# Optimization experiments

Measured on AMD Instinct MI355X. Metric: run time of the kernel, lower is better.

Reference implementation:

```python
import jax, jax.numpy as jnp
import numpy as np

N_WIN, P, C = 2048, 64, 256      # total windows, tokens per window (8x8 partition), channels
M_SEL, KEEP, REAL = 1536, 48, 40 # selected windows, topk tokens kept per window, real (non-padded)
H, DH = 8, 32                    # heads, dim_head
EPS = 1e-5


def _ln(x, g, b):
    mu = jnp.mean(x, axis=-1, keepdims=True)
    v = jnp.mean(jnp.square(x - mu), axis=-1, keepdims=True)
    return (x - mu) * jax.lax.rsqrt(v + EPS) * g + b


def setup_inputs() -> dict:
    key = jax.random.key(0)
    ks = jax.random.split(key, 6)
    rng = np.random.default_rng(0)
    # distinct selected windows
    index_window = jnp.asarray(np.sort(rng.choice(N_WIN, size=M_SEL, replace=False)), jnp.int32)
    # per selected window: 48 distinct token positions out of 64; first 40 real, last 8 padded
    pos = np.argsort(rng.random((M_SEL, P)), axis=1)[:, :KEEP]
    tok = np.arange(M_SEL)[:, None] * P + pos           # flat rows into (M*P, C)
    index_token = jnp.asarray(tok.reshape(-1), jnp.int32)
    asy_index = jnp.asarray(tok[:, :REAL].reshape(-1), jnp.int32)
    padding_index = jnp.asarray(tok[:, REAL:].reshape(-1), jnp.int32)
    w = lambda k, s: jax.random.normal(k, s, jnp.float32) * 0.02
    return {
        "x": jax.random.normal(ks[0], (N_WIN, P, C), jnp.float32),
        "qkv_w": w(ks[1], (C, 3 * C)), "qkv_b": jnp.zeros((3 * C,), jnp.float32),
        "proj_w": w(ks[2], (C, C)), "proj_b": jnp.zeros((C,), jnp.float32),
        "norm1_g": jnp.ones((C,), jnp.float32), "norm1_b": jnp.zeros((C,), jnp.float32),
        "norm2_g": jnp.ones((C,), jnp.float32), "norm2_b": jnp.zeros((C,), jnp.float32),
        "ls1_g": jnp.full((C,), 1e-5, jnp.float32), "ls2_g": jnp.full((C,), 1e-5, jnp.float32),
        "mlp_w1": w(ks[3], (C, 4 * C)), "mlp_b1": jnp.zeros((4 * C,), jnp.float32),
        "mlp_w2": w(ks[4], (4 * C, C)), "mlp_b2": jnp.zeros((C,), jnp.float32),
        "index_window": index_window, "index_token": index_token,
        "padding_index": padding_index, "asy_index": asy_index,
        "M": M_SEL,
    }


def reference(x, qkv_w, qkv_b, proj_w, proj_b, norm1_g, norm1_b, norm2_g, norm2_b,
              ls1_g, ls2_g, mlp_w1, mlp_b1, mlp_w2, mlp_b2,
              index_window, index_token, padding_index, asy_index, M):
    scale = DH ** -0.5
    x1 = _ln(x, norm1_g, norm1_b)                       # norm1 over all windows (N,P,C)
    X = x1
    XX = x1[index_window].reshape(-1, C)                # gather selected windows -> (M*P, C)
    XX = XX.at[asy_index].set(_ln(XX[asy_index], norm2_g, norm2_b))
    shortcut = XX[asy_index]
    xt = XX[index_token].reshape(M, KEEP, C)            # gather kept tokens per window
    qkv = (xt @ qkv_w + qkv_b).reshape(M, KEEP, H, 3 * DH).transpose(0, 2, 1, 3)
    q, k, v = jnp.split(qkv, 3, axis=-1)                # each (M,H,KEEP,DH)
    attn = jnp.einsum('mhqd,mhkd->mhqk', q, k) * scale  # (M,H,Q,K)
    # scatter scores into full map keyed by KEY token row, mask padded keys, gather back
    am = attn.transpose(0, 3, 2, 1).reshape(M * KEEP, KEEP, H)
    attn_map = jnp.zeros((M * P, KEEP, H), attn.dtype)
    attn_map = attn_map.at[index_token].set(am)
    attn_map = attn_map.at[padding_index].set(-10000.0)
    attn = attn_map[index_token].reshape(M, KEEP, KEEP, H).transpose(0, 3, 2, 1)
    attn = jax.nn.softmax(attn, axis=-1)
    out = jnp.einsum('mhqk,mhkd->mhqd', attn, v).transpose(0, 2, 1, 3).reshape(M, KEEP, C)
    out = out @ proj_w + proj_b
    XX = XX.at[index_token].set(out.reshape(-1, C))
    xa = shortcut + XX[asy_index] * ls1_g               # residual + LayerScale
    hdn = jax.nn.gelu(xa @ mlp_w1 + mlp_b1, approximate=False)
    xa = xa + (hdn @ mlp_w2 + mlp_b2) * ls2_g           # (enable_CB=False path)
    XX = XX.at[asy_index].set(xa)
    Xw = X[index_window].reshape(-1, C)
    XX = XX.at[padding_index].set(Xw[padding_index])    # restore padded rows
    X = X.at[index_window].set(XX.reshape(M, P, C))     # scatter windows back
    return X
```

## Files before the change

### kernel.cpp

```cpp
#include <hip/hip_runtime.h>

typedef __attribute__((ext_vector_type(8))) short bf16x8;
typedef __attribute__((ext_vector_type(4))) float f32x4;
typedef unsigned short u16;
typedef unsigned int u32;
typedef unsigned char u8;

#define NWIN 2048
#define P 64
#define C 256
#define MSEL 1536
#define KEEP 48
#define REAL 40
#define H 8
#define DH 32
#define MROWS (MSEL * REAL)

#define B_WQKVT   0
#define B_W1T     393216
#define B_PROJT8  917504
#define B_W2T8    983040
#define B_INV     1245184
#define B_ABUF    1769472
#define B_XA      33226752
#define B_QKV8    64684032
#define B_ATTNO8  111869952
#define B_H8      64684032

__device__ __forceinline__ u16 f2bf(float f) {
    u32 u = __float_as_uint(f);
    u += 0x7FFF + ((u >> 16) & 1);
    return (u16)(u >> 16);
}
__device__ __forceinline__ float bf2f(u16 h) { return __uint_as_float(((u32)h) << 16); }
__device__ __forceinline__ u8 f2fp8(float f) {
    return (u8)__builtin_amdgcn_cvt_pk_fp8_f32(f, 0.0f, 0, false);
}

__global__ __launch_bounds__(256) void prep_weights(const float* __restrict__ qkv_w,
                                                    const float* __restrict__ proj_w,
                                                    const float* __restrict__ w1,
                                                    const float* __restrict__ w2,
                                                    u8* __restrict__ ws) {
    int i = blockIdx.x * 256 + threadIdx.x;
    if (i < 196608) {
        int n = i >> 8, k = i & 255;
        ((u16*)(ws + B_WQKVT))[i] = f2bf(qkv_w[k * 768 + n]);
    } else if (i < 458752) {
        int j = i - 196608; int n = j >> 8, k = j & 255;
        ((u16*)(ws + B_W1T))[j] = f2bf(w1[k * 1024 + n]);
    } else if (i < 524288) {
        int j = i - 458752; int n = j >> 8, k = j & 255;
        (ws + B_PROJT8)[j] = f2fp8(proj_w[k * 256 + n]);
    } else if (i < 786432) {
        int j = i - 524288; int n = j >> 10, k = j & 1023;
        (ws + B_W2T8)[j] = f2fp8(w2[k * 256 + n]);
    } else {
        ((int*)(ws + B_INV))[i - 786432] = -1;
    }
}

__global__ __launch_bounds__(256) void build_inv(const int* __restrict__ asy,
                                                 const int* __restrict__ iwin,
                                                 int* __restrict__ inv) {
    int r = blockIdx.x * 256 + threadIdx.x;
    int flat = asy[r];
    inv[iwin[flat >> 6] * P + (flat & 63)] = r;
}

__global__ __launch_bounds__(256) void ln12_kernel(const float* __restrict__ x,
                                                   const float* __restrict__ g1,
                                                   const float* __restrict__ b1,
                                                   const float* __restrict__ g2,
                                                   const float* __restrict__ b2,
                                                   const int* __restrict__ inv,
                                                   float* __restrict__ out,
                                                   u16* __restrict__ Abuf) {
    int row = blockIdx.x * 4 + (threadIdx.x >> 6);
    int l = threadIdx.x & 63;
    const float4 v = *(const float4*)(x + (size_t)row * C + l * 4);
    float s = v.x + v.y + v.z + v.w;
    float q = v.x * v.x + v.y * v.y + v.z * v.z + v.w * v.w;
    #pragma unroll
    for (int m = 1; m < 64; m <<= 1) { s += __shfl_xor(s, m); q += __shfl_xor(q, m); }
    float mu = s * (1.0f / C);
    float rs = rsqrtf(q * (1.0f / C) - mu * mu + 1e-5f);
    float4 gg = *(const float4*)(g1 + l * 4);
    float4 bb = *(const float4*)(b1 + l * 4);
    float4 o;
    o.x = (v.x - mu) * rs * gg.x + bb.x;
    o.y = (v.y - mu) * rs * gg.y + bb.y;
    o.z = (v.z - mu) * rs * gg.z + bb.z;
    o.w = (v.w - mu) * rs * gg.w + bb.w;
    *(float4*)(out + (size_t)row * C + l * 4) = o;
    int r = inv[row];
    if (r >= 0) {
        float s2 = o.x + o.y + o.z + o.w;
        float q2 = o.x * o.x + o.y * o.y + o.z * o.z + o.w * o.w;
        #pragma unroll
        for (int m = 1; m < 64; m <<= 1) { s2 += __shfl_xor(s2, m); q2 += __shfl_xor(q2, m); }
        float mu2 = s2 * (1.0f / C);
        float rs2 = rsqrtf(q2 * (1.0f / C) - mu2 * mu2 + 1e-5f);
        float4 g2v = *(const float4*)(g2 + l * 4);
        float4 b2v = *(const float4*)(b2 + l * 4);
        ushort4 ob;
        ob.x = f2bf((o.x - mu2) * rs2 * g2v.x + b2v.x);
        ob.y = f2bf((o.y - mu2) * rs2 * g2v.y + b2v.y);
        ob.z = f2bf((o.z - mu2) * rs2 * g2v.z + b2v.z);
        ob.w = f2bf((o.w - mu2) * rs2 * g2v.w + b2v.w);
        *(ushort4*)(Abuf + (size_t)r * C + l * 4) = ob;
    }
}

template <int N, int K, class Epi>
__global__ __launch_bounds__(256) void gemm_bt(const u16* __restrict__ A,
                                               const u16* __restrict__ B, Epi epi,
                                               int chunk) {
    constexpr int NB = N / 128;
    int bid = blockIdx.x;
    bid = (bid & 7) * chunk + (bid >> 3);
    int bm = bid / NB, bn = bid % NB;
    __shared__ u16 lA[128 * 64], lB[128 * 64];
    int t = threadIdx.x;
    int l = t & 63, w = t >> 6;
    int wr = w >> 1, wc = w & 1;
    int l15 = l & 15, g4 = l >> 4;
    int xr = l15 & 7;

    f32x4 acc[4][4];
    #pragma unroll
    for (int a = 0; a < 4; a++)
        #pragma unroll
        for (int bb = 0; bb < 4; bb++)
            #pragma unroll
            for (int i = 0; i < 4; i++) acc[a][bb][i] = 0.0f;

    int rbase = w * 32 + (l >> 3);
    int cg = (l & 7) ^ (l >> 3);
    const u16* gA = A + (size_t)(bm * 128 + rbase) * K + cg * 8;
    const u16* gB = B + (size_t)(bn * 128 + rbase) * K + cg * 8;

    for (int k0 = 0; k0 < K; k0 += 64) {
        __syncthreads();
        #pragma unroll
        for (int j = 0; j < 4; j++)
            __builtin_amdgcn_global_load_lds(
                (const __attribute__((address_space(1))) u32*)(gA + (size_t)j * 8 * K + k0),
                (__attribute__((address_space(3))) u32*)(lA + w * 2048 + j * 512), 16, 0, 0);
        #pragma unroll
        for (int j = 0; j < 4; j++)
            __builtin_amdgcn_global_load_lds(
                (const __attribute__((address_space(1))) u32*)(gB + (size_t)j * 8 * K + k0),
                (__attribute__((address_space(3))) u32*)(lB + w * 2048 + j * 512), 16, 0, 0);
        __syncthreads();
        #pragma unroll
        for (int kk = 0; kk < 2; kk++) {
            bf16x8 af[4], bfr[4];
            #pragma unroll
            for (int mt = 0; mt < 4; mt++)
                af[mt] = *(const bf16x8*)(lA + (wr * 64 + mt * 16 + l15) * 64
                                             + ((kk * 4 + g4) ^ xr) * 8);
            #pragma unroll
            for (int nt = 0; nt < 4; nt++)
                bfr[nt] = *(const bf16x8*)(lB + (wc * 64 + nt * 16 + l15) * 64
                                              + ((kk * 4 + g4) ^ xr) * 8);
            #pragma unroll
            for (int mt = 0; mt < 4; mt++)
                #pragma unroll
                for (int nt = 0; nt < 4; nt++)
                    acc[mt][nt] = __builtin_amdgcn_mfma_f32_16x16x32_bf16(af[mt], bfr[nt], acc[mt][nt], 0, 0, 0);
        }
    }
    int orow = bm * 128 + wr * 64, ocol = bn * 128 + wc * 64;
    #pragma unroll
    for (int mt = 0; mt < 4; mt++)
        #pragma unroll
        for (int nt = 0; nt < 4; nt++)
            #pragma unroll
            for (int rg = 0; rg < 4; rg++)
                epi(orow + mt * 16 + g4 * 4 + rg, ocol + nt * 16 + l15, acc[mt][nt][rg]);
}

template <int N, int K, class Epi>
__global__ __launch_bounds__(256) void gemm_bt8(const u8* __restrict__ A,
                                                const u8* __restrict__ B, Epi epi,
                                                int chunk) {
    constexpr int NB = N / 128;
    int bid = blockIdx.x;
    bid = (bid & 7) * chunk + (bid >> 3);
    int bm = bid / NB, bn = bid % NB;
    __shared__ u8 lA[128 * 64], lB[128 * 64];
    int t = threadIdx.x;
    int l = t & 63, w = t >> 6;
    int wr = w >> 1, wc = w & 1;
    int l15 = l & 15, g4 = l >> 4;
    int xr3 = l15 & 3;

    f32x4 acc[4][4];
    #pragma unroll
    for (int a = 0; a < 4; a++)
        #pragma unroll
        for (int bb = 0; bb < 4; bb++)
            #pragma unroll
            for (int i = 0; i < 4; i++) acc[a][bb][i] = 0.0f;

    int rbase = w * 32 + (l >> 2);
    int sx = (l & 3) ^ ((l >> 2) & 3);
    const u8* gA = A + (size_t)(bm * 128 + rbase) * K + sx * 16;
    const u8* gB = B + (size_t)(bn * 128 + rbase) * K + sx * 16;

    for (int k0 = 0; k0 < K; k0 += 64) {
        __syncthreads();
        #pragma unroll
        for (int j = 0; j < 2; j++)
            __builtin_amdgcn_global_load_lds(
                (const __attribute__((address_space(1))) u32*)(gA + (size_t)j * 16 * K + k0),
                (__attribute__((address_space(3))) u32*)(lA + w * 2048 + j * 1024), 16, 0, 0);
        #pragma unroll
        for (int j = 0; j < 2; j++)
            __builtin_amdgcn_global_load_lds(
                (const __attribute__((address_space(1))) u32*)(gB + (size_t)j * 16 * K + k0),
                (__attribute__((address_space(3))) u32*)(lB + w * 2048 + j * 1024), 16, 0, 0);
        __syncthreads();
        #pragma unroll
        for (int kk = 0; kk < 2; kk++) {
            long af[4], bfr[4];
            #pragma unroll
            for (int mt = 0; mt < 4; mt++) {
                int r = wr * 64 + mt * 16 + l15;
                af[mt] = *(const long*)(lA + r * 64 + (((kk * 2) + (g4 >> 1)) ^ xr3) * 16 + (g4 & 1) * 8);
            }
            #pragma unroll
            for (int nt = 0; nt < 4; nt++) {
                int r = wc * 64 + nt * 16 + l15;
                bfr[nt] = *(const long*)(lB + r * 64 + (((kk * 2) + (g4 >> 1)) ^ xr3) * 16 + (g4 & 1) * 8);
            }
            #pragma unroll
            for (int mt = 0; mt < 4; mt++)
                #pragma unroll
                for (int nt = 0; nt < 4; nt++)
                    acc[mt][nt] = __builtin_amdgcn_mfma_f32_16x16x32_fp8_fp8(af[mt], bfr[nt], acc[mt][nt], 0, 0, 0);
        }
    }
    int orow = bm * 128 + wr * 64, ocol = bn * 128 + wc * 64;
    #pragma unroll
    for (int mt = 0; mt < 4; mt++)
        #pragma unroll
        for (int nt = 0; nt < 4; nt++)
            #pragma unroll
            for (int rg = 0; rg < 4; rg++)
                epi(orow + mt * 16 + g4 * 4 + rg, ocol + nt * 16 + l15, acc[mt][nt][rg]);
}

struct EpiQKV8 {
    const float* bias; u8* out;
    __device__ void operator()(int r, int c, float v) const {
        out[(size_t)r * 768 + c] = f2fp8(v + bias[c]);
    }
};
struct EpiProj {
    const float* bias; const float* ls1; const u16* Abuf; u16* xa;
    __device__ void operator()(int r, int c, float v) const {
        float val = bf2f(Abuf[(size_t)r * 256 + c]) + (v + bias[c]) * ls1[c];
        xa[(size_t)r * 256 + c] = f2bf(val);
    }
};
struct EpiMLP1 {
    const float* bias; u8* h;
    __device__ void operator()(int r, int c, float v) const {
        float x = v + bias[c];
        float u = 0.7978845608f * (x + 0.044715f * x * x * x);
        float e = __expf(2.0f * u);
        h[(size_t)r * 1024 + c] = f2fp8(x - x / (e + 1.0f));
    }
};
struct EpiMLP2 {
    const float* bias; const float* ls2; const u16* xa;
    const int* asy; const int* iwin; float* out;
    __device__ void operator()(int r, int c, float v) const {
        float val = bf2f(xa[(size_t)r * 256 + c]) + (v + bias[c]) * ls2[c];
        int flat = asy[r];
        out[((size_t)iwin[flat >> 6] * P + (flat & 63)) * C + c] = val;
    }
};

__global__ __launch_bounds__(256) void attn_kernel(const u8* __restrict__ QKV,
                                                   u8* __restrict__ out) {
    __shared__ u8 lds[4 * (48 * 80 + 32 * 80)];
    int m = blockIdx.x;
    int t = threadIdx.x, l = t & 63, w = t >> 6;
    int l15 = l & 15, g4 = l >> 4;
    u8* Pb = lds + w * (48 * 80 + 32 * 80);
    u8* Vt = Pb + 48 * 80;

    u32* z = (u32*)Pb;
    for (int i = l; i < (48 * 80 + 32 * 80) / 4; i += 64) z[i] = 0;

    const float scale = 0.17677669529663687f;

    for (int hh = 0; hh < 2; hh++) {
        int h = w + hh * 4;
        const u8* base = QKV + (size_t)m * REAL * 768 + h * 96;

        for (int i = l; i < REAL * 8; i += 64) {
            int kk = i >> 3, dg = i & 7;
            u32 vv = *(const u32*)(base + (size_t)kk * 768 + 64 + dg * 4);
            #pragma unroll
            for (int j = 0; j < 4; j++) Vt[(dg * 4 + j) * 80 + kk] = (u8)(vv >> (j * 8));
        }

        long qf[3], kf[3];
        #pragma unroll
        for (int mt = 0; mt < 3; mt++) {
            int q = mt * 16 + l15;
            qf[mt] = (q < REAL) ? *(const long*)(base + (size_t)q * 768 + g4 * 8) : 0L;
        }
        #pragma unroll
        for (int nt = 0; nt < 3; nt++) {
            int kk = nt * 16 + l15;
            kf[nt] = (kk < REAL) ? *(const long*)(base + (size_t)kk * 768 + 32 + g4 * 8) : 0L;
        }
        f32x4 s[3][3];
        #pragma unroll
        for (int a = 0; a < 3; a++)
            #pragma unroll
            for (int bb = 0; bb < 3; bb++)
                #pragma unroll
                for (int i = 0; i < 4; i++) s[a][bb][i] = 0.0f;
        #pragma unroll
        for (int mt = 0; mt < 3; mt++)
            #pragma unroll
            for (int nt = 0; nt < 3; nt++)
                s[mt][nt] = __builtin_amdgcn_mfma_f32_16x16x32_fp8_fp8(qf[mt], kf[nt], s[mt][nt], 0, 0, 0);

        #pragma unroll
        for (int mt = 0; mt < 3; mt++) {
            #pragma unroll
            for (int rg = 0; rg < 4; rg++) {
                float v0 = s[mt][0][rg] * scale;
                float v1 = s[mt][1][rg] * scale;
                float v2 = s[mt][2][rg] * scale;
                bool k2ok = (32 + l15) < REAL;
                float mx = fmaxf(fmaxf(v0, v1), k2ok ? v2 : -1e30f);
                #pragma unroll
                for (int xm = 1; xm < 16; xm <<= 1) mx = fmaxf(mx, __shfl_xor(mx, xm));
                float e0 = __expf(v0 - mx);
                float e1 = __expf(v1 - mx);
                float e2 = k2ok ? __expf(v2 - mx) : 0.0f;
                float sm = e0 + e1 + e2;
                #pragma unroll
                for (int xm = 1; xm < 16; xm <<= 1) sm += __shfl_xor(sm, xm);
                float inv = 1.0f / sm;
                int q = mt * 16 + g4 * 4 + rg;
                Pb[q * 80 + l15]      = f2fp8(e0 * inv);
                Pb[q * 80 + 16 + l15] = f2fp8(e1 * inv);
                Pb[q * 80 + 32 + l15] = k2ok ? f2fp8(e2 * inv) : (u8)0;
            }
        }

        f32x4 o[3][2];
        #pragma unroll
        for (int a = 0; a < 3; a++)
            #pragma unroll
            for (int bb = 0; bb < 2; bb++)
                #pragma unroll
                for (int i = 0; i < 4; i++) o[a][bb][i] = 0.0f;
        #pragma unroll
        for (int kt = 0; kt < 2; kt++) {
            long pf[3], vf[2];
            #pragma unroll
            for (int mt = 0; mt < 3; mt++)
                pf[mt] = *(const long*)(Pb + (mt * 16 + l15) * 80 + kt * 32 + g4 * 8);
            #pragma unroll
            for (int nt = 0; nt < 2; nt++)
                vf[nt] = *(const long*)(Vt + (nt * 16 + l15) * 80 + kt * 32 + g4 * 8);
            #pragma unroll
            for (int mt = 0; mt < 3; mt++)
                #pragma unroll
                for (int nt = 0; nt < 2; nt++)
                    o[mt][nt] = __builtin_amdgcn_mfma_f32_16x16x32_fp8_fp8(pf[mt], vf[nt], o[mt][nt], 0, 0, 0);
        }
        #pragma unroll
        for (int mt = 0; mt < 3; mt++)
            #pragma unroll
            for (int nt = 0; nt < 2; nt++)
                #pragma unroll
                for (int rg = 0; rg < 4; rg++) {
                    int q = mt * 16 + g4 * 4 + rg;
                    if (q < REAL)
                        out[((size_t)m * REAL + q) * C + h * DH + nt * 16 + l15] = f2fp8(o[mt][nt][rg]);
                }
    }
}

extern "C" void kernel_launch(void* const* d_in, const int* in_sizes, int n_in,
                              void* d_out, int out_size, void* d_ws, size_t ws_size,
                              hipStream_t stream) {
    const float* x      = (const float*)d_in[0];
    const float* qkv_w  = (const float*)d_in[1];
    const float* qkv_b  = (const float*)d_in[2];
    const float* proj_w = (const float*)d_in[3];
    const float* proj_b = (const float*)d_in[4];
    const float* n1g    = (const float*)d_in[5];
    const float* n1b    = (const float*)d_in[6];
    const float* n2g    = (const float*)d_in[7];
    const float* n2b    = (const float*)d_in[8];
    const float* ls1    = (const float*)d_in[9];
    const float* ls2    = (const float*)d_in[10];
    const float* w1     = (const float*)d_in[11];
    const float* b1     = (const float*)d_in[12];
    const float* w2     = (const float*)d_in[13];
    const float* b2     = (const float*)d_in[14];
    const int*   iwin   = (const int*)d_in[15];
    const int*   asy    = (const int*)d_in[18];
    float* out = (float*)d_out;
    u8* ws = (u8*)d_ws;

    u16* WqkvT  = (u16*)(ws + B_WQKVT);
    u16* W1T    = (u16*)(ws + B_W1T);
    u8*  ProjT8 = ws + B_PROJT8;
    u8*  W2T8   = ws + B_W2T8;
    int* inv    = (int*)(ws + B_INV);
    u16* Abuf   = (u16*)(ws + B_ABUF);
    u16* XA     = (u16*)(ws + B_XA);
    u8*  QKV8   = ws + B_QKV8;
    u8*  AttnO8 = ws + B_ATTNO8;
    u8*  H8     = ws + B_H8;

    prep_weights<<<3584, 256, 0, stream>>>(qkv_w, proj_w, w1, w2, ws);
    build_inv<<<240, 256, 0, stream>>>(asy, iwin, inv);
    ln12_kernel<<<(NWIN * P) / 4, 256, 0, stream>>>(x, n1g, n1b, n2g, n2b, inv, out, Abuf);
    {
        int nwg = (MROWS / 128) * 6;
        gemm_bt<768, 256, EpiQKV8><<<nwg, 256, 0, stream>>>(Abuf, WqkvT, EpiQKV8{qkv_b, QKV8}, nwg / 8);
    }
    attn_kernel<<<MSEL, 256, 0, stream>>>(QKV8, AttnO8);
    {
        int nwg = (MROWS / 128) * 2;
        gemm_bt8<256, 256, EpiProj><<<nwg, 256, 0, stream>>>(AttnO8, ProjT8, EpiProj{proj_b, ls1, Abuf, XA}, nwg / 8);
    }
    {
        int nwg = (MROWS / 128) * 8;
        gemm_bt<1024, 256, EpiMLP1><<<nwg, 256, 0, stream>>>(XA, W1T, EpiMLP1{b1, H8}, nwg / 8);
    }
    {
        int nwg = (MROWS / 128) * 2;
        gemm_bt8<256, 1024, EpiMLP2><<<nwg, 256, 0, stream>>>(H8, W2T8, EpiMLP2{b2, ls2, XA, asy, iwin, out}, nwg / 8);
    }
}
```

Measured before the change: 575.0 us.

## Vectorize GEMM and attention epilogue stores via permuted fp8 layouts and cheaper GELU

GEMM epilogues move from per-element callbacks to per-tile store methods. Bias and LayerScale values are hoisted, and adjacent fp8 outputs are packed into 16- or 32-bit stores. The column order of the packed QKV, attention and MLP1 outputs is permuted to make this possible, and the proj and W2 weights are reordered in prep to cancel the permutation. GELU switches to the sigmoid approximation x*sigmoid(1.702x), which is less accurate than the tanh form. LN1 now skips writing rows that the MLP path overwrites later.

Measured after the change: 476.3 us. -17.2%, faster.

```diff
diff --git a/kernel.cpp b/kernel.cpp
--- a/kernel.cpp
+++ b/kernel.cpp
@@ -36,6 +36,10 @@
 __device__ __forceinline__ u8 f2fp8(float f) {
     return (u8)__builtin_amdgcn_cvt_pk_fp8_f32(f, 0.0f, 0, false);
 }
+__device__ __forceinline__ float gelu_s(float x) {
+    return x * __builtin_amdgcn_rcpf(1.0f + __expf(-1.702f * x));
+}
+__device__ __forceinline__ int pinv32(int s) { return (s & 1) * 16 + (s >> 1); }
 
 __global__ __launch_bounds__(256) void prep_weights(const float* __restrict__ qkv_w,
                                                     const float* __restrict__ proj_w,
@@ -50,10 +54,14 @@
         int j = i - 196608; int n = j >> 8, k = j & 255;
         ((u16*)(ws + B_W1T))[j] = f2bf(w1[k * 1024 + n]);
     } else if (i < 524288) {
-        int j = i - 458752; int n = j >> 8, k = j & 255;
-        (ws + B_PROJT8)[j] = f2fp8(proj_w[k * 256 + n]);
+        int j = i - 458752; int n = j >> 8, rk = j & 255;
+        int h = rk >> 5, s = rk & 31;
+        int d = pinv32(pinv32(s));
+        (ws + B_PROJT8)[j] = f2fp8(proj_w[(h * 32 + d) * 256 + n]);
     } else if (i < 786432) {
-        int j = i - 524288; int n = j >> 10, k = j & 1023;
+        int j = i - 524288; int n = j >> 10, ks = j & 1023;
+        int grp = ks >> 6, pos = ks & 63;
+        int k = grp * 64 + (pos & 3) * 16 + (pos >> 2);
         (ws + B_W2T8)[j] = f2fp8(w2[k * 256 + n]);
     } else {
         ((int*)(ws + B_INV))[i - 786432] = -1;
@@ -92,9 +100,10 @@
     o.y = (v.y - mu) * rs * gg.y + bb.y;
     o.z = (v.z - mu) * rs * gg.z + bb.z;
     o.w = (v.w - mu) * rs * gg.w + bb.w;
-    *(float4*)(out + (size_t)row * C + l * 4) = o;
     int r = inv[row];
-    if (r >= 0) {
+    if (r < 0) {
+        *(float4*)(out + (size_t)row * C + l * 4) = o;
+    } else {
         float s2 = o.x + o.y + o.z + o.w;
         float q2 = o.x * o.x + o.y * o.y + o.z * o.z + o.w * o.w;
         #pragma unroll
@@ -171,14 +180,7 @@
                     acc[mt][nt] = __builtin_amdgcn_mfma_f32_16x16x32_bf16(af[mt], bfr[nt], acc[mt][nt], 0, 0, 0);
         }
     }
-    int orow = bm * 128 + wr * 64, ocol = bn * 128 + wc * 64;
-    #pragma unroll
-    for (int mt = 0; mt < 4; mt++)
-        #pragma unroll
-        for (int nt = 0; nt < 4; nt++)
-            #pragma unroll
-            for (int rg = 0; rg < 4; rg++)
-                epi(orow + mt * 16 + g4 * 4 + rg, ocol + nt * 16 + l15, acc[mt][nt][rg]);
+    epi.store(bm * 128 + wr * 64, bn * 128 + wc * 64, l15, g4, acc);
 }
 
 template <int N, int K, class Epi>
@@ -242,45 +244,97 @@
                     acc[mt][nt] = __builtin_amdgcn_mfma_f32_16x16x32_fp8_fp8(af[mt], bfr[nt], acc[mt][nt], 0, 0, 0);
         }
     }
-    int orow = bm * 128 + wr * 64, ocol = bn * 128 + wc * 64;
-    #pragma unroll
-    for (int mt = 0; mt < 4; mt++)
-        #pragma unroll
-        for (int nt = 0; nt < 4; nt++)
-            #pragma unroll
-            for (int rg = 0; rg < 4; rg++)
-                epi(orow + mt * 16 + g4 * 4 + rg, ocol + nt * 16 + l15, acc[mt][nt][rg]);
+    epi.store(bm * 128 + wr * 64, bn * 128 + wc * 64, l15, g4, acc);
 }
 
 struct EpiQKV8 {
     const float* bias; u8* out;
-    __device__ void operator()(int r, int c, float v) const {
-        out[(size_t)r * 768 + c] = f2fp8(v + bias[c]);
+    __device__ void store(int orow, int ocol, int l15, int g4, const f32x4 (&acc)[4][4]) const {
+        float b[4];
+        #pragma unroll
+        for (int nt = 0; nt < 4; nt++) b[nt] = bias[ocol + nt * 16 + l15];
+        #pragma unroll
+        for (int mt = 0; mt < 4; mt++)
+            #pragma unroll
+            for (int rg = 0; rg < 4; rg++) {
+                int r = orow + mt * 16 + g4 * 4 + rg;
+                #pragma unroll
+                for (int np = 0; np < 2; np++) {
+                    u32 t = __builtin_amdgcn_cvt_pk_fp8_f32(
+                        acc[mt][np * 2][rg] + b[np * 2],
+                        acc[mt][np * 2 + 1][rg] + b[np * 2 + 1], 0, false);
+                    *(u16*)(out + (size_t)r * 768 + ocol + np * 32 + l15 * 2) = (u16)t;
+                }
+            }
+    }
+};
+struct EpiMLP1 {
+    const float* bias; u8* h;
+    __device__ void store(int orow, int ocol, int l15, int g4, const f32x4 (&acc)[4][4]) const {
+        float b[4];
+        #pragma unroll
+        for (int nt = 0; nt < 4; nt++) b[nt] = bias[ocol + nt * 16 + l15];
+        #pragma unroll
+        for (int mt = 0; mt < 4; mt++)
+            #pragma unroll
+            for (int rg = 0; rg < 4; rg++) {
+                int r = orow + mt * 16 + g4 * 4 + rg;
+                float g0 = gelu_s(acc[mt][0][rg] + b[0]);
+                float g1 = gelu_s(acc[mt][1][rg] + b[1]);
+                float g2 = gelu_s(acc[mt][2][rg] + b[2]);
+                float g3 = gelu_s(acc[mt][3][rg] + b[3]);
+                u32 v = __builtin_amdgcn_cvt_pk_fp8_f32(g0, g1, 0, false);
+                v = (u32)__builtin_amdgcn_cvt_pk_fp8_f32(g2, g3, (int)v, true);
+                *(u32*)(h + (size_t)r * 1024 + ocol + l15 * 4) = v;
+            }
     }
 };
 struct EpiProj {
     const float* bias; const float* ls1; const u16* Abuf; u16* xa;
-    __device__ void operator()(int r, int c, float v) const {
-        float val = bf2f(Abuf[(size_t)r * 256 + c]) + (v + bias[c]) * ls1[c];
-        xa[(size_t)r * 256 + c] = f2bf(val);
-    }
-};
-struct EpiMLP1 {
-    const float* bias; u8* h;
-    __device__ void operator()(int r, int c, float v) const {
-        float x = v + bias[c];
-        float u = 0.7978845608f * (x + 0.044715f * x * x * x);
-        float e = __expf(2.0f * u);
-        h[(size_t)r * 1024 + c] = f2fp8(x - x / (e + 1.0f));
+    __device__ void store(int orow, int ocol, int l15, int g4, const f32x4 (&acc)[4][4]) const {
+        float pb[4], l1[4];
+        #pragma unroll
+        for (int nt = 0; nt < 4; nt++) {
+            int c = ocol + nt * 16 + l15;
+            pb[nt] = bias[c]; l1[nt] = ls1[c];
+        }
+        #pragma unroll
+        for (int mt = 0; mt < 4; mt++)
+            #pragma unroll
+            for (int rg = 0; rg < 4; rg++) {
+                int r = orow + mt * 16 + g4 * 4 + rg;
+                #pragma unroll
+                for (int nt = 0; nt < 4; nt++) {
+                    int c = ocol + nt * 16 + l15;
+                    float val = bf2f(Abuf[(size_t)r * 256 + c]) + (acc[mt][nt][rg] + pb[nt]) * l1[nt];
+                    xa[(size_t)r * 256 + c] = f2bf(val);
+                }
+            }
     }
 };
 struct EpiMLP2 {
     const float* bias; const float* ls2; const u16* xa;
     const int* asy; const int* iwin; float* out;
-    __device__ void operator()(int r, int c, float v) const {
-        float val = bf2f(xa[(size_t)r * 256 + c]) + (v + bias[c]) * ls2[c];
-        int flat = asy[r];
-        out[((size_t)iwin[flat >> 6] * P + (flat & 63)) * C + c] = val;
+    __device__ void store(int orow, int ocol, int l15, int g4, const f32x4 (&acc)[4][4]) const {
+        float b[4], l2[4];
+        #pragma unroll
+        for (int nt = 0; nt < 4; nt++) {
+            int c = ocol + nt * 16 + l15;
+            b[nt] = bias[c]; l2[nt] = ls2[c];
+        }
+        #pragma unroll
+        for (int mt = 0; mt < 4; mt++)
+            #pragma unroll
+            for (int rg = 0; rg < 4; rg++) {
+                int r = orow + mt * 16 + g4 * 4 + rg;
+                int flat = asy[r];
+                size_t ob = ((size_t)iwin[flat >> 6] * P + (flat & 63)) * C;
+                #pragma unroll
+                for (int nt = 0; nt < 4; nt++) {
+                    int c = ocol + nt * 16 + l15;
+                    out[ob + c] = bf2f(xa[(size_t)r * 256 + c]) + (acc[mt][nt][rg] + b[nt]) * l2[nt];
+                }
+            }
     }
 };
 
@@ -383,13 +437,13 @@
         #pragma unroll
         for (int mt = 0; mt < 3; mt++)
             #pragma unroll
-            for (int nt = 0; nt < 2; nt++)
-                #pragma unroll
-                for (int rg = 0; rg < 4; rg++) {
-                    int q = mt * 16 + g4 * 4 + rg;
-                    if (q < REAL)
-                        out[((size_t)m * REAL + q) * C + h * DH + nt * 16 + l15] = f2fp8(o[mt][nt][rg]);
+            for (int rg = 0; rg < 4; rg++) {
+                int q = mt * 16 + g4 * 4 + rg;
+                if (q < REAL) {
+                    u32 tt = __builtin_amdgcn_cvt_pk_fp8_f32(o[mt][0][rg], o[mt][1][rg], 0, false);
+                    *(u16*)(out + ((size_t)m * REAL + q) * 256 + h * 32 + l15 * 2) = (u16)tt;
                 }
+            }
     }
 }
 
```
